# Optimization experiments

Hardware: AMD Instinct MI355X
Metric: run time of the kernel (lower is better)

Reference implementation:

```python
import jax, jax.numpy as jnp
import numpy as np

GS = 7          # grid size
NB = 2          # boxes per cell
NC = 20         # classes
LAMBDA_COORD = 0.5
LAMBDA_NOOBJ = 0.5


def setup_inputs() -> dict:
    key = jax.random.key(0)
    k1, k2, k3 = jax.random.split(key, 3)
    B = 8192
    C = 5 * NB + NC  # 30
    inputs = jax.random.uniform(k1, (B, GS, GS, C), minval=0.05, maxval=0.95, dtype=jnp.float32)
    targets = jax.random.uniform(k2, (B, GS, GS, C), minval=0.05, maxval=0.95, dtype=jnp.float32)
    obj = jax.random.bernoulli(k3, 0.15, (B, GS, GS)).astype(jnp.float32)
    # _transform_targets writes the SAME box into both box slots and sets conf=1 for obj cells
    targets = targets.at[..., 5:9].set(targets[..., 0:4])
    targets = targets.at[..., 4].set(obj)
    targets = targets.at[..., 9].set(obj)
    return {"inputs": inputs, "targets": targets}


def _yolo_loss(inputs, targets):
    bs = inputs.shape[0]
    gs = inputs.shape[2]
    dt = inputs.dtype

    conf_t = targets[..., 4]
    coord = (conf_t > 0).astype(dt)          # [B,S,S] cells containing an object
    noobj = (conf_t == 0).astype(dt)          # [B,S,S]

    # ---- no-object confidence loss: channels 4 + 5*b for each box b ----
    conf_idx = jnp.arange(NB) * 5 + 4         # [4, 9]
    pc = inputs[..., conf_idx]                # [B,S,S,NB]
    tc = targets[..., conf_idx]
    loss_noobj = jnp.sum(noobj[..., None] * (pc - tc) ** 2)

    # ---- per-cell box matching (vectorizes the pairwise IoU loop) ----
    bp = inputs[..., :5 * NB].reshape(inputs.shape[:3] + (NB, 5))    # [B,S,S,NB,5]
    # original takes boxes_targets[i] (first box of the pair; both slots are identical)
    bt = targets[..., :5 * NB].reshape(targets.shape[:3] + (NB, 5))[..., 0, :]  # [B,S,S,5]

    def to_xyxy(b):
        # faithful to original: xy scaled by 1/gs, wh NOT scaled
        xy = b[..., :2] / gs
        wh = b[..., 2:4]
        return jnp.concatenate([xy - 0.5 * wh, xy + 0.5 * wh], axis=-1)

    pxy = to_xyxy(bp)                          # [B,S,S,NB,4]
    txy = to_xyxy(bt)[..., None, :]            # [B,S,S,1,4]
    lt = jnp.maximum(pxy[..., :2], txy[..., :2])
    rb = jnp.minimum(pxy[..., 2:], txy[..., 2:])
    whi = jnp.clip(rb - lt, 0.0)
    inter = whi[..., 0] * whi[..., 1]          # [B,S,S,NB]
    area = lambda x: (x[..., 2] - x[..., 0]) * (x[..., 3] - x[..., 1])
    iou = inter / (area(pxy) + area(txy) - inter)   # [B,S,S,NB]

    max_iou = jnp.max(iou, axis=-1)            # [B,S,S]
    idx = jnp.argmax(iou, axis=-1)             # [B,S,S] responsible box (first max, like torch)
    idx_b = jnp.broadcast_to(idx[..., None, None], idx.shape + (1, 5))
    rp = jnp.take_along_axis(bp, idx_b, axis=-2)[..., 0, :]  # [B,S,S,5] responsible preds

    loss_xy = jnp.sum(coord[..., None] * (rp[..., :2] - bt[..., :2]) ** 2)
    loss_wh = jnp.sum(coord[..., None] * (jnp.sqrt(rp[..., 2:4]) - jnp.sqrt(bt[..., 2:4])) ** 2)
    loss_obj = jnp.sum(coord * (rp[..., 4] - max_iou) ** 2)
    loss_class = jnp.sum(coord[..., None] * (inputs[..., 5 * NB:] - targets[..., 5 * NB:]) ** 2)

    loss_boxes = LAMBDA_COORD * (loss_xy + loss_wh) / bs
    loss_conf = (loss_obj + LAMBDA_NOOBJ * loss_noobj) / bs
    loss_class = loss_class / bs
    return loss_boxes, loss_conf, loss_class


def reference(inputs, targets):
    return _yolo_loss(inputs, targets)
```

## Files before the change

### kernel.cpp

```cpp
#include <hip/hip_runtime.h>

#define CC 30
#define TPW 64
#define HALF 32
#define WPB 4
#define HALF_FLOATS (HALF * CC)
#define HALF_VEC4   (HALF_FLOATS / 4)

#define AS1 __attribute__((address_space(1)))
#define AS3 __attribute__((address_space(3)))

__device__ __forceinline__ void dma16(const float4* gsrc_lane, float4* lds_base) {
    __builtin_amdgcn_global_load_lds((const AS1 unsigned int*)gsrc_lane,
                                     (AS3 unsigned int*)lds_base, 16, 0, 0);
}

__device__ __forceinline__ void prefetch_half(const float* __restrict__ in,
                                              const float* __restrict__ tg,
                                              size_t cell_base,
                                              float* lin, float* ltg, int lane) {
    const float4* gin = (const float4*)(in + cell_base * CC);
    const float4* gtg = (const float4*)(tg + cell_base * CC);
    float4* vin = (float4*)lin;
    float4* vtg = (float4*)ltg;
    #pragma unroll
    for (int k = 0; k < 3; ++k) {
        dma16(gin + k * 64 + lane, vin + k * 64);
        dma16(gtg + k * 64 + lane, vtg + k * 64);
    }
    if (lane < 48) {
        dma16(gin + 192 + lane, vin + 192);
        dma16(gtg + 192 + lane, vtg + 192);
    }
}

__device__ __forceinline__ void compute_half(const float* __restrict__ lin,
                                             const float* __restrict__ ltg,
                                             int lane, float inv_gs,
                                             float& a_boxes, float& a_conf, float& a_class) {
    const int c = lane >> 1;
    const int h = lane & 1;
    const float* f = lin + c * CC;
    const float* t = ltg + c * CC;

    const int hb = 5 * h;
    const float px  = f[hb + 0];
    const float py  = f[hb + 1];
    const float pw  = f[hb + 2];
    const float phh = f[hb + 3];
    const float pc  = f[hb + 4];

    const float bt0 = t[0], bt1 = t[1], bt2 = t[2], bt3 = t[3];
    const float conf_t  = t[4];
    const float tconf_h = f == t ? 0.0f : t[hb + 4];
    const float coord = (conf_t > 0.0f)  ? 1.0f : 0.0f;
    const float noobj = (conf_t == 0.0f) ? 1.0f : 0.0f;

    const float dn = pc - tconf_h;

    const float ttx = bt0 * inv_gs, tty = bt1 * inv_gs;
    const float txmin = ttx - 0.5f * bt2, tymin = tty - 0.5f * bt3;
    const float txmax = ttx + 0.5f * bt2, tymax = tty + 0.5f * bt3;
    const float tarea = (txmax - txmin) * (tymax - tymin);

    const float cx = px * inv_gs, cy = py * inv_gs;
    const float xmin = cx - 0.5f * pw, ymin = cy - 0.5f * phh;
    const float xmax = cx + 0.5f * pw, ymax = cy + 0.5f * phh;
    const float wx = fmaxf(fminf(xmax, txmax) - fmaxf(xmin, txmin), 0.0f);
    const float wy = fmaxf(fminf(ymax, tymax) - fmaxf(ymin, tymin), 0.0f);
    const float inter = wx * wy;
    const float parea = (xmax - xmin) * (ymax - ymin);
    const float iou_mine = inter / (parea + tarea - inter);

    const float iou_other = __shfl_xor(iou_mine, 1, 64);
    const float iou0 = h ? iou_other : iou_mine;
    const float iou1 = h ? iou_mine  : iou_other;
    const bool  sel1 = iou1 > iou0;
    const float max_iou = fmaxf(iou0, iou1);
    const float own = ((h == 1) == sel1) ? 1.0f : 0.0f;

    const float dx = px - bt0, dy = py - bt1;
    const float sw = sqrtf(pw)  - sqrtf(bt2);
    const float sh = sqrtf(phh) - sqrtf(bt3);
    const float dob = pc - max_iou;

    a_boxes += own * coord * (dx * dx + dy * dy + sw * sw + sh * sh);
    a_conf  += own * coord * (dob * dob) + 0.5f * noobj * dn * dn;

    const float2* f2 = (const float2*)f;
    const float2* t2 = (const float2*)t;
    float l = 0.0f;
    #pragma unroll
    for (int j = 0; j < 5; ++j) {
        const float2 fv = f2[5 + 5 * h + j];
        const float2 tv = t2[5 + 5 * h + j];
        const float gx = fv.x - tv.x;
        const float gy = fv.y - tv.y;
        l += gx * gx + gy * gy;
    }
    a_class += coord * l;
}

__device__ __forceinline__ void cell_losses_global(const float* __restrict__ f,
                                                   const float* __restrict__ t,
                                                   float& o_boxes, float& o_conf, float& o_cls) {
    const float inv_gs = 0.14285714285714285f;
    const float conf_t = t[4];
    const float coord  = (conf_t > 0.0f)  ? 1.0f : 0.0f;
    const float noobj  = (conf_t == 0.0f) ? 1.0f : 0.0f;
    const float d0 = f[4] - t[4];
    const float d1 = f[9] - t[9];
    const float l_noobj = noobj * (d0 * d0 + d1 * d1);
    const float bt0 = t[0], bt1 = t[1], bt2 = t[2], bt3 = t[3];
    const float ttx = bt0 * inv_gs, tty = bt1 * inv_gs;
    const float txmin = ttx - 0.5f * bt2, tymin = tty - 0.5f * bt3;
    const float txmax = ttx + 0.5f * bt2, tymax = tty + 0.5f * bt3;
    const float tarea = (txmax - txmin) * (tymax - tymin);
    float iou0, iou1;
    {
        const float cx = f[0] * inv_gs, cy = f[1] * inv_gs;
        const float xmin = cx - 0.5f * f[2], ymin = cy - 0.5f * f[3];
        const float xmax = cx + 0.5f * f[2], ymax = cy + 0.5f * f[3];
        const float wx = fmaxf(fminf(xmax, txmax) - fmaxf(xmin, txmin), 0.0f);
        const float wy = fmaxf(fminf(ymax, tymax) - fmaxf(ymin, tymin), 0.0f);
        const float inter = wx * wy;
        const float parea = (xmax - xmin) * (ymax - ymin);
        iou0 = inter / (parea + tarea - inter);
    }
    {
        const float cx = f[5] * inv_gs, cy = f[6] * inv_gs;
        const float xmin = cx - 0.5f * f[7], ymin = cy - 0.5f * f[8];
        const float xmax = cx + 0.5f * f[7], ymax = cy + 0.5f * f[8];
        const float wx = fmaxf(fminf(xmax, txmax) - fmaxf(xmin, txmin), 0.0f);
        const float wy = fmaxf(fminf(ymax, tymax) - fmaxf(ymin, tymin), 0.0f);
        const float inter = wx * wy;
        const float parea = (xmax - xmin) * (ymax - ymin);
        iou1 = inter / (parea + tarea - inter);
    }
    const bool  sel1    = iou1 > iou0;
    const float max_iou = fmaxf(iou0, iou1);
    const float rp0 = sel1 ? f[5] : f[0];
    const float rp1 = sel1 ? f[6] : f[1];
    const float rp2 = sel1 ? f[7] : f[2];
    const float rp3 = sel1 ? f[8] : f[3];
    const float rp4 = sel1 ? f[9] : f[4];
    const float dx = rp0 - bt0, dy = rp1 - bt1;
    const float sw = sqrtf(rp2) - sqrtf(bt2);
    const float sh = sqrtf(rp3) - sqrtf(bt3);
    const float dob = rp4 - max_iou;
    float l_cls = 0.0f;
    #pragma unroll
    for (int j = 10; j < 30; ++j) {
        const float d = f[j] - t[j];
        l_cls += d * d;
    }
    o_boxes += coord * (dx * dx + dy * dy + sw * sw + sh * sh);
    o_conf  += coord * (dob * dob) + 0.5f * l_noobj;
    o_cls   += coord * l_cls;
}

__global__ __launch_bounds__(256) void yolo_main(
        const float* __restrict__ in,
        const float* __restrict__ tg,
        float* __restrict__ ws,
        int ncells, int nwaves_total, int pstride) {
    __shared__ float s_lds[WPB * 2 * 2 * HALF_FLOATS];

    const int tid   = threadIdx.x;
    const int lane  = tid & 63;
    const int wave  = tid >> 6;
    const int gwave = blockIdx.x * WPB + wave;

    float* base = s_lds + wave * (2 * 2 * HALF_FLOATS);
    float* bin[2] = { base,                    base + 2 * HALF_FLOATS };
    float* btg[2] = { base + HALF_FLOATS,      base + 3 * HALF_FLOATS };

    const int nfull = ncells / TPW;
    const float inv_gs = 0.14285714285714285f;

    float a_boxes = 0.0f, a_conf = 0.0f, a_class = 0.0f;

    int ct = gwave;
    if (ct < nfull) {
        prefetch_half(in, tg, (size_t)ct * TPW, bin[0], btg[0], lane);
        int chalf = 0;
        int cur = 0;
        while (true) {
            int nt = ct, nh = chalf + 1;
            if (nh == 2) { nh = 0; nt = ct + nwaves_total; }
            const bool has_next = (nt < nfull);

            asm volatile("s_waitcnt lgkmcnt(0)" ::: "memory");
            __builtin_amdgcn_wave_barrier();
            if (has_next)
                prefetch_half(in, tg, (size_t)nt * TPW + (size_t)nh * HALF,
                              bin[cur ^ 1], btg[cur ^ 1], lane);
            __builtin_amdgcn_wave_barrier();
            if (has_next) asm volatile("s_waitcnt vmcnt(8)" ::: "memory");
            else          asm volatile("s_waitcnt vmcnt(0)" ::: "memory");
            __builtin_amdgcn_wave_barrier();
            compute_half(bin[cur], btg[cur], lane, inv_gs, a_boxes, a_conf, a_class);
            __builtin_amdgcn_wave_barrier();

            if (!has_next) break;
            ct = nt; chalf = nh; cur ^= 1;
        }
    }

    #pragma unroll
    for (int off = 32; off > 0; off >>= 1) {
        a_boxes += __shfl_down(a_boxes, off, 64);
        a_conf  += __shfl_down(a_conf,  off, 64);
        a_class += __shfl_down(a_class, off, 64);
    }
    if (lane == 0) {
        ws[gwave]               = a_boxes;
        ws[gwave + pstride]     = a_conf;
        ws[gwave + 2 * pstride] = a_class;
    }
}

__global__ __launch_bounds__(256) void yolo_finalize(
        const float* __restrict__ in,
        const float* __restrict__ tg,
        const float* __restrict__ ws, float* __restrict__ out,
        int nparts, int pstride, int rem_base, int rem, float inv_bs) {
    float b = 0.0f, c = 0.0f, k = 0.0f;
    for (int i = threadIdx.x; i < nparts; i += 256) {
        b += ws[i];
        c += ws[i + pstride];
        k += ws[i + 2 * pstride];
    }
    if ((int)threadIdx.x < rem) {
        const size_t cell = (size_t)(rem_base + threadIdx.x) * CC;
        cell_losses_global(in + cell, tg + cell, b, c, k);
    }
    #pragma unroll
    for (int off = 32; off > 0; off >>= 1) {
        b += __shfl_down(b, off, 64);
        c += __shfl_down(c, off, 64);
        k += __shfl_down(k, off, 64);
    }
    __shared__ float s_red[4][3];
    const int wave = threadIdx.x >> 6;
    if ((threadIdx.x & 63) == 0) {
        s_red[wave][0] = b;
        s_red[wave][1] = c;
        s_red[wave][2] = k;
    }
    __syncthreads();
    if (threadIdx.x == 0) {
        const float tb = s_red[0][0] + s_red[1][0] + s_red[2][0] + s_red[3][0];
        const float tc = s_red[0][1] + s_red[1][1] + s_red[2][1] + s_red[3][1];
        const float tk = s_red[0][2] + s_red[1][2] + s_red[2][2] + s_red[3][2];
        out[0] = 0.5f * tb * inv_bs;
        out[1] = tc * inv_bs;
        out[2] = tk * inv_bs;
    }
}

extern "C" void kernel_launch(void* const* d_in, const int* in_sizes, int n_in,
                              void* d_out, int out_size, void* d_ws, size_t ws_size,
                              hipStream_t stream) {
    const float* in = (const float*)d_in[0];
    const float* tg = (const float*)d_in[1];
    float* out = (float*)d_out;
    float* ws  = (float*)d_ws;

    const int ncells = in_sizes[0] / CC;
    const int B = ncells / 49;
    const float inv_bs = 1.0f / (float)B;

    const int nblocks = 512;
    const int nwaves  = nblocks * WPB;
    const int pstride = nwaves;
    const int nfull   = ncells / TPW;
    const int rem     = ncells - nfull * TPW;

    yolo_main<<<nblocks, 256, 0, stream>>>(in, tg, ws, ncells, nwaves, pstride);
    yolo_finalize<<<1, 256, 0, stream>>>(in, tg, ws, out, nwaves, pstride,
                                         nfull * TPW, rem, inv_bs);
}
```

Before: 115.5 us.

## Replace per-wave double-buffered LDS prefetch with single-buffer loop and more blocks

Drops the software double-buffering, in which each wave prefetched the next half-tile into LDS while computing the current one. Each wave now loads a 32-cell tile, waits for it, and computes it. The grid goes from 512 to 1280 blocks, so latency is hidden by more resident waves and higher occupancy rather than by explicit pipelining. Per-wave LDS use halves, but each wave now stalls fully on every load, and more partial sums reach the finalize kernel.

```diff
diff --git a/kernel.cpp b/kernel.cpp
--- a/kernel.cpp
+++ b/kernel.cpp
@@ -1,11 +1,10 @@
 #include <hip/hip_runtime.h>
 
 #define CC 30
-#define TPW 64
-#define HALF 32
+#define TPW 32
 #define WPB 4
-#define HALF_FLOATS (HALF * CC)
-#define HALF_VEC4   (HALF_FLOATS / 4)
+#define TILE_FLOATS (TPW * CC)
+#define TILE_VEC4   (TILE_FLOATS / 4)
 
 #define AS1 __attribute__((address_space(1)))
 #define AS3 __attribute__((address_space(3)))
@@ -15,7 +14,7 @@
                                      (AS3 unsigned int*)lds_base, 16, 0, 0);
 }
 
-__device__ __forceinline__ void prefetch_half(const float* __restrict__ in,
+__device__ __forceinline__ void prefetch_tile(const float* __restrict__ in,
                                               const float* __restrict__ tg,
                                               size_t cell_base,
                                               float* lin, float* ltg, int lane) {
@@ -34,7 +33,7 @@
     }
 }
 
-__device__ __forceinline__ void compute_half(const float* __restrict__ lin,
+__device__ __forceinline__ void compute_tile(const float* __restrict__ lin,
                                              const float* __restrict__ ltg,
                                              int lane, float inv_gs,
                                              float& a_boxes, float& a_conf, float& a_class) {
@@ -52,7 +51,7 @@
 
     const float bt0 = t[0], bt1 = t[1], bt2 = t[2], bt3 = t[3];
     const float conf_t  = t[4];
-    const float tconf_h = f == t ? 0.0f : t[hb + 4];
+    const float tconf_h = t[hb + 4];
     const float coord = (conf_t > 0.0f)  ? 1.0f : 0.0f;
     const float noobj = (conf_t == 0.0f) ? 1.0f : 0.0f;
 
@@ -164,47 +163,29 @@
         const float* __restrict__ tg,
         float* __restrict__ ws,
         int ncells, int nwaves_total, int pstride) {
-    __shared__ float s_lds[WPB * 2 * 2 * HALF_FLOATS];
+    __shared__ float s_lds[WPB * 2 * TILE_FLOATS];
 
     const int tid   = threadIdx.x;
     const int lane  = tid & 63;
     const int wave  = tid >> 6;
     const int gwave = blockIdx.x * WPB + wave;
 
-    float* base = s_lds + wave * (2 * 2 * HALF_FLOATS);
-    float* bin[2] = { base,                    base + 2 * HALF_FLOATS };
-    float* btg[2] = { base + HALF_FLOATS,      base + 3 * HALF_FLOATS };
-
-    const int nfull = ncells / TPW;
+    float* lin = s_lds + wave * (2 * TILE_FLOATS);
+    float* ltg = lin + TILE_FLOATS;
+
+    const int ntiles = ncells / TPW;
     const float inv_gs = 0.14285714285714285f;
 
     float a_boxes = 0.0f, a_conf = 0.0f, a_class = 0.0f;
 
-    int ct = gwave;
-    if (ct < nfull) {
-        prefetch_half(in, tg, (size_t)ct * TPW, bin[0], btg[0], lane);
-        int chalf = 0;
-        int cur = 0;
-        while (true) {
-            int nt = ct, nh = chalf + 1;
-            if (nh == 2) { nh = 0; nt = ct + nwaves_total; }
-            const bool has_next = (nt < nfull);
-
-            asm volatile("s_waitcnt lgkmcnt(0)" ::: "memory");
-            __builtin_amdgcn_wave_barrier();
-            if (has_next)
-                prefetch_half(in, tg, (size_t)nt * TPW + (size_t)nh * HALF,
-                              bin[cur ^ 1], btg[cur ^ 1], lane);
-            __builtin_amdgcn_wave_barrier();
-            if (has_next) asm volatile("s_waitcnt vmcnt(8)" ::: "memory");
-            else          asm volatile("s_waitcnt vmcnt(0)" ::: "memory");
-            __builtin_amdgcn_wave_barrier();
-            compute_half(bin[cur], btg[cur], lane, inv_gs, a_boxes, a_conf, a_class);
-            __builtin_amdgcn_wave_barrier();
-
-            if (!has_next) break;
-            ct = nt; chalf = nh; cur ^= 1;
-        }
+    for (int t = gwave; t < ntiles; t += nwaves_total) {
+        asm volatile("s_waitcnt lgkmcnt(0)" ::: "memory");
+        __builtin_amdgcn_wave_barrier();
+        prefetch_tile(in, tg, (size_t)t * TPW, lin, ltg, lane);
+        asm volatile("s_waitcnt vmcnt(0)" ::: "memory");
+        __builtin_amdgcn_wave_barrier();
+        compute_tile(lin, ltg, lane, inv_gs, a_boxes, a_conf, a_class);
+        __builtin_amdgcn_wave_barrier();
     }
 
     #pragma unroll
@@ -271,13 +252,13 @@
     const int B = ncells / 49;
     const float inv_bs = 1.0f / (float)B;
 
-    const int nblocks = 512;
+    const int nblocks = 1280;
     const int nwaves  = nblocks * WPB;
     const int pstride = nwaves;
-    const int nfull   = ncells / TPW;
-    const int rem     = ncells - nfull * TPW;
+    const int ntiles  = ncells / TPW;
+    const int rem     = ncells - ntiles * TPW;
 
     yolo_main<<<nblocks, 256, 0, stream>>>(in, tg, ws, ncells, nwaves, pstride);
     yolo_finalize<<<1, 256, 0, stream>>>(in, tg, ws, out, nwaves, pstride,
-                                         nfull * TPW, rem, inv_bs);
-}
+                                         ntiles * TPW, rem, inv_bs);
+}
```

New measurement: 117.3 us. No clear change (+1.6%).
